# Kernel tuning notes

Measured on AMD Instinct MI355X. Metric: run time of the kernel, lower is better.

The kernel has to match this reference:

```python
import jax, jax.numpy as jnp
import numpy as np

T, B, H, V, L = 1024, 16, 1024, 100, 3


def setup_inputs() -> dict:
    key = jax.random.key(0)
    k_x, k_e, k_w, k_b = jax.random.split(key, 4)
    x = jax.random.randint(k_x, (T, B), 0, V)                      # [T, B] token ids
    emb = jax.random.normal(k_e, (V, H), dtype=jnp.float32) * 0.1  # embedding table
    # per-layer Linear(H, 3H): stacked weights/biases (all layers have in=out=H)
    W = jax.random.normal(k_w, (L, H, 3 * H), dtype=jnp.float32) * (1.0 / np.sqrt(H))
    b = jax.random.normal(k_b, (L, 3 * H), dtype=jnp.float32) * 0.01
    return {"x": x, "emb": emb, "W": W, "b": b}


def _qrnn_layer(h, W_l, b_l):
    # h: [T, B, H] -> gates [T, B, 3H]
    g = jnp.einsum("tbh,hk->tbk", h, W_l) + b_l
    z, f, o = jnp.split(g, 3, axis=-1)
    z = jnp.tanh(z)
    f = jax.nn.sigmoid(f)
    o = jax.nn.sigmoid(o)

    def step(c, zf):
        z_t, f_t = zf
        c = f_t * z_t + (1.0 - f_t) * c  # forget-mult recurrence
        return c, c

    c0 = jnp.zeros(h.shape[1:], dtype=h.dtype)  # hidden init is None -> zeros
    _, C = jax.lax.scan(step, c0, (z, f))       # C: [T, B, H]
    return o * C


def reference(x, emb, W, b):
    h = emb[x]  # [T, B, H]
    for l in range(L):
        h = _qrnn_layer(h, W[l], b[l])
    return h[:-1]  # drop last timestep, [T-1, B, H]
```

## Files before the change

### kernel.cpp

```cpp
#include <hip/hip_runtime.h>
#include <hip/hip_bf16.h>
#include <hip/hip_cooperative_groups.h>

namespace coop = cooperative_groups;

#define T_DIM 1024
#define B_DIM 16
#define H_DIM 1024
#define L_DIM 3
#define M_DIM (T_DIM * B_DIM)
#define N_DIM (3 * H_DIM)
#define K_DIM H_DIM
#define NC 64
#define CS 16

typedef __bf16 bf16x8 __attribute__((ext_vector_type(8)));
typedef __bf16 bf16x4 __attribute__((ext_vector_type(4)));
typedef _Float16 half4 __attribute__((ext_vector_type(4)));
typedef float f32x4 __attribute__((ext_vector_type(4)));

__device__ __forceinline__ __bf16 f2bf(float f) {
    return (__bf16)__float2bfloat16(f);
}

__device__ __forceinline__ void async_cp16(const void* g, void* lds) {
    __builtin_amdgcn_global_load_lds(
        (__attribute__((address_space(1))) void*)g,
        (__attribute__((address_space(3))) void*)lds, 16, 0, 0);
}

#define TW_BLOCKS (32 * 96 * 3)
__global__ void prep_kernel(const float* __restrict__ W, __bf16* __restrict__ Wt,
                            const int* __restrict__ x, const float4* __restrict__ emb,
                            __bf16* __restrict__ h) {
    if (blockIdx.x < TW_BLOCKS) {
        __shared__ __bf16 tile[32][33];
        const int blk = blockIdx.x;
        const int l = blk / 3072;
        const int r2 = blk % 3072;
        const int n0 = (r2 / 32) * 32, k0 = (r2 % 32) * 32;
        const int tx = threadIdx.x & 31, ty = threadIdx.x >> 5;
        const float* Wl = W + (size_t)l * K_DIM * N_DIM;
        __bf16* Wtl = Wt + (size_t)l * N_DIM * K_DIM;
#pragma unroll
        for (int q = 0; q < 4; q++) {
            int k = ty + q * 8;
            tile[k][tx] = f2bf(Wl[(size_t)(k0 + k) * N_DIM + n0 + tx]);
        }
        __syncthreads();
#pragma unroll
        for (int q = 0; q < 4; q++) {
            int n = ty + q * 8;
            Wtl[(size_t)(n0 + n) * K_DIM + k0 + tx] = tile[tx][n];
        }
    } else {
        int i = (blockIdx.x - TW_BLOCKS) * 256 + threadIdx.x;
        int row = i >> 8;
        int j = i & 255;
        int idx = x[row];
        float4 v = emb[(size_t)idx * 256 + j];
        __bf16* dst = h + (size_t)row * H_DIM + j * 4;
        dst[0] = f2bf(v.x); dst[1] = f2bf(v.y); dst[2] = f2bf(v.z); dst[3] = f2bf(v.w);
    }
}

__global__ __launch_bounds__(256, 2) void gemm_gates(
    const __bf16* __restrict__ A,
    const __bf16* __restrict__ Wt,
    const float* __restrict__ bias,
    _Float16* __restrict__ Gz, _Float16* __restrict__ Gf, _Float16* __restrict__ Go) {
    __shared__ __align__(16) __bf16 As[128 * 64];
    __shared__ __align__(16) __bf16 Bs[128 * 64];

    const int tid = threadIdx.x;
    const int wid = tid >> 6, lane = tid & 63;
    const int bm = blockIdx.x, bn = blockIdx.y;
    const int waveM = wid >> 1, waveN = wid & 1;
    const int lm = lane & 15, kg = lane >> 4;

    int roff[4], loff[4];
#pragma unroll
    for (int q = 0; q < 4; q++) {
        int cell = q * 256 + tid;
        int r = cell >> 3, s = cell & 7;
        int g = s ^ (r & 7);
        roff[q] = r * K_DIM + g * 8;
        loff[q] = (q * 256 + wid * 64) * 8;
    }

    const __bf16* Abase = A + (size_t)(bm * 128) * K_DIM;
    const __bf16* Bbase = Wt + (size_t)(bn * 128) * K_DIM;

    f32x4 acc[4][4] = {};

    for (int k0 = 0; k0 < K_DIM; k0 += 64) {
#pragma unroll
        for (int q = 0; q < 4; q++)
            async_cp16(Abase + k0 + roff[q], As + loff[q]);
#pragma unroll
        for (int q = 0; q < 4; q++)
            async_cp16(Bbase + k0 + roff[q], Bs + loff[q]);
        __syncthreads();

#pragma unroll
        for (int h = 0; h < 2; h++) {
            const int cs = ((h * 4 + kg) ^ (lane & 7)) * 8;
            bf16x8 af[4], bf[4];
#pragma unroll
            for (int i = 0; i < 4; i++)
                af[i] = *(const bf16x8*)(As + (waveM * 64 + i * 16 + lm) * 64 + cs);
#pragma unroll
            for (int j = 0; j < 4; j++)
                bf[j] = *(const bf16x8*)(Bs + (waveN * 64 + j * 16 + lm) * 64 + cs);
#pragma unroll
            for (int i = 0; i < 4; i++)
#pragma unroll
                for (int j = 0; j < 4; j++)
                    acc[i][j] = __builtin_amdgcn_mfma_f32_16x16x32_bf16(af[i], bf[j], acc[i][j], 0, 0, 0);
        }
        __syncthreads();
    }

    const int plane = bn >> 3;
    _Float16* __restrict__ P = (plane == 0) ? Gz : (plane == 1) ? Gf : Go;
#pragma unroll
    for (int i = 0; i < 4; i++) {
#pragma unroll
        for (int j = 0; j < 4; j++) {
            int ncol = bn * 128 + waveN * 64 + j * 16 + lm;
            int col = ncol & 1023;
            float bv = bias[ncol];
#pragma unroll
            for (int r = 0; r < 4; r++) {
                int mrow = bm * 128 + waveM * 64 + i * 16 + kg * 4 + r;
                float g = acc[i][j][r] + bv;
                float val;
                if (plane == 0) {
                    float e = __expf(-2.0f * fabsf(g));
                    float rc = __builtin_amdgcn_rcpf(1.0f + e);
                    val = copysignf(fmaf(-2.0f * e, rc, 1.0f), g);
                } else {
                    float e = __expf(-g);
                    val = __builtin_amdgcn_rcpf(1.0f + e);
                }
                P[(size_t)mrow * H_DIM + col] = (_Float16)val;
            }
        }
    }
}

__global__ __launch_bounds__(256, 4) void scan_fused(
    const _Float16* __restrict__ Gz, const _Float16* __restrict__ Gf,
    const _Float16* __restrict__ Go,
    float* __restrict__ cA, float* __restrict__ cM,
    __bf16* __restrict__ hdst, float* __restrict__ fdst, int is_last) {
    int tidg = blockIdx.x * 256 + threadIdx.x;
    int ci = tidg >> 12;
    int chg = tidg & 4095;
    size_t base = (size_t)(ci * CS) * 16384 + (size_t)chg * 4;

    half4 zs[CS], fs[CS];
    f32x4 Aacc = {0.f, 0.f, 0.f, 0.f};
    f32x4 Macc = {1.f, 1.f, 1.f, 1.f};
    {
        size_t p = base;
#pragma unroll
        for (int s = 0; s < CS; s++) {
            zs[s] = *(const half4*)(Gz + p);
            fs[s] = *(const half4*)(Gf + p);
#pragma unroll
            for (int k = 0; k < 4; k++) {
                float fk = (float)fs[s][k], zk = (float)zs[s][k];
                Aacc[k] = fk * zk + (1.f - fk) * Aacc[k];
                Macc[k] = (1.f - fk) * Macc[k];
            }
            p += 16384;
        }
    }
    size_t idx = (size_t)ci * 16384 + (size_t)chg * 4;
    *(f32x4*)(cA + idx) = Aacc;
    *(f32x4*)(cM + idx) = Macc;

    __threadfence();
    coop::this_grid().sync();

    f32x4 c = {0.f, 0.f, 0.f, 0.f};
    for (int cj = 0; cj < ci; cj++) {
        size_t jdx = (size_t)cj * 16384 + (size_t)chg * 4;
        f32x4 a = *(const f32x4*)(cA + jdx);
        f32x4 m = *(const f32x4*)(cM + jdx);
#pragma unroll
        for (int k = 0; k < 4; k++) c[k] = a[k] + m[k] * c[k];
    }

    size_t p = base;
#pragma unroll
    for (int s = 0; s < CS; s++) {
        int t = ci * CS + s;
        half4 o = *(const half4*)(Go + p);
        f32x4 val;
#pragma unroll
        for (int k = 0; k < 4; k++) {
            float fk = (float)fs[s][k];
            c[k] = fk * (float)zs[s][k] + (1.f - fk) * c[k];
            val[k] = (float)o[k] * c[k];
        }
        if (is_last) {
            if (t < T_DIM - 1)
                *(f32x4*)(fdst + p) = val;
        } else {
            bf16x4 hv;
#pragma unroll
            for (int k = 0; k < 4; k++) hv[k] = f2bf(val[k]);
            *(bf16x4*)(hdst + p) = hv;
        }
        p += 16384;
    }
}

__global__ __launch_bounds__(256, 8) void scan_pass1(
    const _Float16* __restrict__ Gz, const _Float16* __restrict__ Gf,
    float* __restrict__ cA, float* __restrict__ cM) {
    int tidg = blockIdx.x * 256 + threadIdx.x;
    int ci = tidg >> 12;
    int chg = tidg & 4095;
    size_t base = (size_t)(ci * CS) * 16384 + (size_t)chg * 4;
    f32x4 Aacc = {0.f, 0.f, 0.f, 0.f};
    f32x4 Macc = {1.f, 1.f, 1.f, 1.f};
#pragma unroll
    for (int s = 0; s < CS; s++) {
        half4 z = *(const half4*)(Gz + base);
        half4 f = *(const half4*)(Gf + base);
#pragma unroll
        for (int k = 0; k < 4; k++) {
            float fk = (float)f[k], zk = (float)z[k];
            Aacc[k] = fk * zk + (1.f - fk) * Aacc[k];
            Macc[k] = (1.f - fk) * Macc[k];
        }
        base += 16384;
    }
    size_t idx = (size_t)ci * 16384 + (size_t)chg * 4;
    *(f32x4*)(cA + idx) = Aacc;
    *(f32x4*)(cM + idx) = Macc;
}

__global__ __launch_bounds__(256, 8) void scan_pass23(
    const _Float16* __restrict__ Gz, const _Float16* __restrict__ Gf,
    const _Float16* __restrict__ Go,
    const float* __restrict__ cA, const float* __restrict__ cM,
    __bf16* __restrict__ hdst, float* __restrict__ fdst, int is_last) {
    int tidg = blockIdx.x * 256 + threadIdx.x;
    int ci = tidg >> 12;
    int chg = tidg & 4095;
    f32x4 c = {0.f, 0.f, 0.f, 0.f};
    for (int cj = 0; cj < ci; cj++) {
        size_t jdx = (size_t)cj * 16384 + (size_t)chg * 4;
        f32x4 a = *(const f32x4*)(cA + jdx);
        f32x4 m = *(const f32x4*)(cM + jdx);
#pragma unroll
        for (int k = 0; k < 4; k++) c[k] = a[k] + m[k] * c[k];
    }
    size_t p = (size_t)(ci * CS) * 16384 + (size_t)chg * 4;
#pragma unroll
    for (int s = 0; s < CS; s++) {
        int t = ci * CS + s;
        half4 z = *(const half4*)(Gz + p);
        half4 f = *(const half4*)(Gf + p);
        half4 o = *(const half4*)(Go + p);
        f32x4 val;
#pragma unroll
        for (int k = 0; k < 4; k++) {
            float fk = (float)f[k];
            c[k] = fk * (float)z[k] + (1.f - fk) * c[k];
            val[k] = (float)o[k] * c[k];
        }
        if (is_last) {
            if (t < T_DIM - 1)
                *(f32x4*)(fdst + p) = val;
        } else {
            bf16x4 hv;
#pragma unroll
            for (int k = 0; k < 4; k++) hv[k] = f2bf(val[k]);
            *(bf16x4*)(hdst + p) = hv;
        }
        p += 16384;
    }
}

extern "C" void kernel_launch(void* const* d_in, const int* in_sizes, int n_in,
                              void* d_out, int out_size, void* d_ws, size_t ws_size,
                              hipStream_t stream) {
    const int* x = (const int*)d_in[0];
    const float* emb = (const float*)d_in[1];
    const float* W = (const float*)d_in[2];
    const float* b = (const float*)d_in[3];
    float* out = (float*)d_out;

    char* ws = (char*)d_ws;
    size_t need = (size_t)L_DIM * N_DIM * K_DIM * 2
                + (size_t)M_DIM * H_DIM * 2
                + 3ull * M_DIM * H_DIM * 2
                + 2ull * NC * 16384 * 4;
    if (ws_size < need) return;

    __bf16* Wt = (__bf16*)ws;     ws += (size_t)L_DIM * N_DIM * K_DIM * 2;
    __bf16* hbuf = (__bf16*)ws;   ws += (size_t)M_DIM * H_DIM * 2;
    _Float16* Gz = (_Float16*)ws; ws += (size_t)M_DIM * H_DIM * 2;
    _Float16* Gf = (_Float16*)ws; ws += (size_t)M_DIM * H_DIM * 2;
    _Float16* Go = (_Float16*)ws; ws += (size_t)M_DIM * H_DIM * 2;
    float* cA = (float*)ws;       ws += (size_t)NC * 16384 * 4;
    float* cM = (float*)ws;

    int blocksPerCU = 0;
    hipError_t qe = hipOccupancyMaxActiveBlocksPerMultiprocessor(
        &blocksPerCU, (const void*)scan_fused, 256, 0);
    const bool use_coop = (qe == hipSuccess && blocksPerCU >= 4);

    prep_kernel<<<TW_BLOCKS + 16384, 256, 0, stream>>>(W, Wt, x, (const float4*)emb, hbuf);

    for (int l = 0; l < L_DIM; l++) {
        gemm_gates<<<dim3(M_DIM / 128, N_DIM / 128), 256, 0, stream>>>(
            hbuf, Wt + (size_t)l * N_DIM * K_DIM, b + (size_t)l * N_DIM, Gz, Gf, Go);
        int last = (l == L_DIM - 1);

        bool launched = false;
        if (use_coop) {
            const _Float16* aGz = Gz; const _Float16* aGf = Gf; const _Float16* aGo = Go;
            float* acA = cA; float* acM = cM;
            __bf16* ah = hbuf; float* af = out;
            void* args[] = {(void*)&aGz, (void*)&aGf, (void*)&aGo,
                            (void*)&acA, (void*)&acM, (void*)&ah, (void*)&af, (void*)&last};
            hipError_t e = hipLaunchCooperativeKernel((const void*)scan_fused,
                                                      dim3(1024), dim3(256), args, 0, stream);
            launched = (e == hipSuccess);
        }
        if (!launched) {
            scan_pass1<<<1024, 256, 0, stream>>>(Gz, Gf, cA, cM);
            scan_pass23<<<1024, 256, 0, stream>>>(Gz, Gf, Go, cA, cM, hbuf, out, last);
        }
    }
}
```

Before: 550.7 us.

## Rewrite gates GEMM as 256x256 tile with multi-stage async LDS pipeline

Replaces the 128x128, 4-wave GEMM with a 256x256 tile, 8-wave kernel. It splits K into 32-wide halves held in a 4-slot LDS ring and interleaves global-to-LDS prefetch with the MFMA phases, using explicit barriers, vmcnt waits and setprio. This targets the synchronous load-then-compute pattern and raises arithmetic intensity per block. In exchange it uses 128 KB of LDS and large accumulator register pressure, which limits occupancy, and the hand-tuned waitcnt schedule is fragile.

```diff
diff --git a/kernel.cpp b/kernel.cpp
--- a/kernel.cpp
+++ b/kernel.cpp
@@ -64,86 +64,129 @@
     }
 }
 
-__global__ __launch_bounds__(256, 2) void gemm_gates(
+__global__ __launch_bounds__(512, 2) void gemm_gates(
     const __bf16* __restrict__ A,
     const __bf16* __restrict__ Wt,
     const float* __restrict__ bias,
     _Float16* __restrict__ Gz, _Float16* __restrict__ Gf, _Float16* __restrict__ Go) {
-    __shared__ __align__(16) __bf16 As[128 * 64];
-    __shared__ __align__(16) __bf16 Bs[128 * 64];
+    __shared__ __align__(16) __bf16 As[4 * 8192];
+    __shared__ __align__(16) __bf16 Bs[4 * 8192];
 
     const int tid = threadIdx.x;
-    const int wid = tid >> 6, lane = tid & 63;
+    const int lane = tid & 63, wid = tid >> 6;
+    const int lm = lane & 15, kg = lane >> 4;
+    const int waveM = wid >> 2, waveN = wid & 3;
     const int bm = blockIdx.x, bn = blockIdx.y;
-    const int waveM = wid >> 1, waveN = wid & 1;
-    const int lm = lane & 15, kg = lane >> 4;
-
-    int roff[4], loff[4];
-#pragma unroll
-    for (int q = 0; q < 4; q++) {
-        int cell = q * 256 + tid;
-        int r = cell >> 3, s = cell & 7;
-        int g = s ^ (r & 7);
-        roff[q] = r * K_DIM + g * 8;
-        loff[q] = (q * 256 + wid * 64) * 8;
-    }
-
-    const __bf16* Abase = A + (size_t)(bm * 128) * K_DIM;
-    const __bf16* Bbase = Wt + (size_t)(bn * 128) * K_DIM;
-
-    f32x4 acc[4][4] = {};
-
-    for (int k0 = 0; k0 < K_DIM; k0 += 64) {
-#pragma unroll
-        for (int q = 0; q < 4; q++)
-            async_cp16(Abase + k0 + roff[q], As + loff[q]);
-#pragma unroll
-        for (int q = 0; q < 4; q++)
-            async_cp16(Bbase + k0 + roff[q], Bs + loff[q]);
-        __syncthreads();
-
-#pragma unroll
-        for (int h = 0; h < 2; h++) {
-            const int cs = ((h * 4 + kg) ^ (lane & 7)) * 8;
-            bf16x8 af[4], bf[4];
-#pragma unroll
-            for (int i = 0; i < 4; i++)
-                af[i] = *(const bf16x8*)(As + (waveM * 64 + i * 16 + lm) * 64 + cs);
-#pragma unroll
-            for (int j = 0; j < 4; j++)
-                bf[j] = *(const bf16x8*)(Bs + (waveN * 64 + j * 16 + lm) * 64 + cs);
-#pragma unroll
-            for (int i = 0; i < 4; i++)
-#pragma unroll
-                for (int j = 0; j < 4; j++)
-                    acc[i][j] = __builtin_amdgcn_mfma_f32_16x16x32_bf16(af[i], bf[j], acc[i][j], 0, 0, 0);
-        }
-        __syncthreads();
-    }
-
-    const int plane = bn >> 3;
+
+    const int sr = tid >> 2;
+    const int sch = (tid & 3) ^ ((sr >> 1) & 3);
+    const int ga0 = sr * K_DIM + sch * 8;
+    const int ga1 = (sr + 128) * K_DIM + sch * 8;
+    const int lo0 = tid * 8;
+    const int lo1 = (512 + tid) * 8;
+
+    const __bf16* Abase = A + (size_t)(bm * 256) * K_DIM;
+    const __bf16* Bbase = Wt + (size_t)(bn * 256) * K_DIM;
+
+    const int slot8 = (kg ^ ((lm >> 1) & 3)) * 8;
+    const int a_off0 = (waveM * 128 + 0 * 16 + lm) * 32 + slot8;
+    const int a_off1 = (waveM * 128 + 1 * 16 + lm) * 32 + slot8;
+    const int a_off2 = (waveM * 128 + 2 * 16 + lm) * 32 + slot8;
+    const int a_off3 = (waveM * 128 + 3 * 16 + lm) * 32 + slot8;
+    const int b_off0 = (waveN * 64 + 0 * 16 + lm) * 32 + slot8;
+    const int b_off1 = (waveN * 64 + 1 * 16 + lm) * 32 + slot8;
+    const int b_off2 = (waveN * 64 + 2 * 16 + lm) * 32 + slot8;
+    const int b_off3 = (waveN * 64 + 3 * 16 + lm) * 32 + slot8;
+
+    f32x4 acc[8][4] = {};
+    bf16x8 af0, af1, af2, af3;
+    bf16x8 bf0 = {}, bf1 = {}, bf2 = {}, bf3 = {};
+
+#define STAGE(ARR, GB, TILE, KH) { \
+    const int tt_ = (TILE) & 15; \
+    const int kc_ = tt_ * 64 + (KH) * 32; \
+    __bf16* dst_ = (ARR) + ((tt_ & 1) * 2 + (KH)) * 8192; \
+    async_cp16((GB) + kc_ + ga0, dst_ + lo0); \
+    async_cp16((GB) + kc_ + ga1, dst_ + lo1); }
+
+#define MF1(IA, J, AF, BF) \
+    acc[IA][J] = __builtin_amdgcn_mfma_f32_16x16x32_bf16(AF, BF, acc[IA][J], 0, 0, 0);
+#define MF4(IA, AF) MF1(IA, 0, AF, bf0) MF1(IA, 1, AF, bf1) MF1(IA, 2, AF, bf2) MF1(IA, 3, AF, bf3)
+
+#define PHASE(BUF, KH, MQ, LB, STG, VM) { \
+    const __bf16* rA_ = As + ((BUF) * 2 + (KH)) * 8192 + (MQ) * 2048; \
+    if (LB) { \
+        const __bf16* rB_ = Bs + ((BUF) * 2 + (KH)) * 8192; \
+        bf0 = *(const bf16x8*)(rB_ + b_off0); \
+        bf1 = *(const bf16x8*)(rB_ + b_off1); \
+        bf2 = *(const bf16x8*)(rB_ + b_off2); \
+        bf3 = *(const bf16x8*)(rB_ + b_off3); } \
+    af0 = *(const bf16x8*)(rA_ + a_off0); \
+    af1 = *(const bf16x8*)(rA_ + a_off1); \
+    af2 = *(const bf16x8*)(rA_ + a_off2); \
+    af3 = *(const bf16x8*)(rA_ + a_off3); \
+    STG; \
+    __builtin_amdgcn_s_barrier(); \
+    asm volatile("s_waitcnt lgkmcnt(0)" ::: "memory"); \
+    __builtin_amdgcn_sched_barrier(0); \
+    __builtin_amdgcn_s_setprio(1); \
+    MF4((MQ) * 4 + 0, af0) MF4((MQ) * 4 + 1, af1) MF4((MQ) * 4 + 2, af2) MF4((MQ) * 4 + 3, af3) \
+    __builtin_amdgcn_s_setprio(0); \
+    __builtin_amdgcn_sched_barrier(0); \
+    if (VM) { asm volatile("s_waitcnt vmcnt(8)" ::: "memory"); } \
+    __builtin_amdgcn_s_barrier(); }
+
+    STAGE(As, Abase, 0, 0) STAGE(Bs, Bbase, 0, 0)
+    STAGE(As, Abase, 0, 1) STAGE(Bs, Bbase, 0, 1)
+    STAGE(As, Abase, 1, 0) STAGE(Bs, Bbase, 1, 0)
+    asm volatile("s_waitcnt vmcnt(8)" ::: "memory");
+    __builtin_amdgcn_s_barrier();
+
+#pragma unroll 1
+    for (int t = 0; t < 16; t += 2) {
+        PHASE(0, 0, 0, 1, STAGE(As, Abase, t + 1, 1), 0)
+        PHASE(0, 0, 1, 0, STAGE(Bs, Bbase, t + 1, 1), 1)
+        PHASE(0, 1, 0, 1, STAGE(As, Abase, t + 2, 0), 0)
+        PHASE(0, 1, 1, 0, STAGE(Bs, Bbase, t + 2, 0), 1)
+        PHASE(1, 0, 0, 1, STAGE(As, Abase, t + 2, 1), 0)
+        PHASE(1, 0, 1, 0, STAGE(Bs, Bbase, t + 2, 1), 1)
+        PHASE(1, 1, 0, 1, STAGE(As, Abase, t + 3, 0), 0)
+        PHASE(1, 1, 1, 0, STAGE(Bs, Bbase, t + 3, 0), 1)
+    }
+    asm volatile("s_waitcnt vmcnt(0)" ::: "memory");
+
+#undef PHASE
+#undef MF4
+#undef MF1
+#undef STAGE
+
+    const int plane = bn >> 2;
     _Float16* __restrict__ P = (plane == 0) ? Gz : (plane == 1) ? Gf : Go;
-#pragma unroll
-    for (int i = 0; i < 4; i++) {
-#pragma unroll
-        for (int j = 0; j < 4; j++) {
-            int ncol = bn * 128 + waveN * 64 + j * 16 + lm;
-            int col = ncol & 1023;
-            float bv = bias[ncol];
-#pragma unroll
-            for (int r = 0; r < 4; r++) {
-                int mrow = bm * 128 + waveM * 64 + i * 16 + kg * 4 + r;
-                float g = acc[i][j][r] + bv;
-                float val;
-                if (plane == 0) {
-                    float e = __expf(-2.0f * fabsf(g));
-                    float rc = __builtin_amdgcn_rcpf(1.0f + e);
-                    val = copysignf(fmaf(-2.0f * e, rc, 1.0f), g);
-                } else {
-                    float e = __expf(-g);
-                    val = __builtin_amdgcn_rcpf(1.0f + e);
+    const int colbase = (bn & 3) * 256 + waveN * 64;
+    const int nb = bn * 256 + waveN * 64;
+#pragma unroll
+    for (int mq = 0; mq < 2; mq++) {
+#pragma unroll
+        for (int i = 0; i < 4; i++) {
+#pragma unroll
+            for (int j = 0; j < 4; j++) {
+                int col = colbase + j * 16 + lm;
+                float bv = bias[nb + j * 16 + lm];
+#pragma unroll
+                for (int r = 0; r < 4; r++) {
+                    int mrow = bm * 256 + waveM * 128 + mq * 64 + i * 16 + kg * 4 + r;
+                    float g = acc[mq * 4 + i][j][r] + bv;
+                    float val;
+                    if (plane == 0) {
+                        float e = __expf(-2.0f * fabsf(g));
+                        float rc = __builtin_amdgcn_rcpf(1.0f + e);
+                        val = copysignf(fmaf(-2.0f * e, rc, 1.0f), g);
+                    } else {
+                        float e = __expf(-g);
+                        val = __builtin_amdgcn_rcpf(1.0f + e);
+                    }
+                    P[(size_t)mrow * H_DIM + col] = (_Float16)val;
                 }
-                P[(size_t)mrow * H_DIM + col] = (_Float16)val;
             }
         }
     }
@@ -319,7 +362,7 @@
     prep_kernel<<<TW_BLOCKS + 16384, 256, 0, stream>>>(W, Wt, x, (const float4*)emb, hbuf);
 
     for (int l = 0; l < L_DIM; l++) {
-        gemm_gates<<<dim3(M_DIM / 128, N_DIM / 128), 256, 0, stream>>>(
+        gemm_gates<<<dim3(M_DIM / 256, N_DIM / 256), 512, 0, stream>>>(
             hbuf, Wt + (size_t)l * N_DIM * K_DIM, b + (size_t)l * N_DIM, Gz, Gf, Go);
         int last = (l == L_DIM - 1);
 
```

Result: no change. 559.7 us (+1.6%).
